# Optimization experiments

Measured on AMD Instinct MI355X. Metric: run time of the kernel, lower is better.

The kernel has to match this reference:

```python
import jax, jax.numpy as jnp
import numpy as np
import math

B, S, D, H = 2, 2048, 1024, 16
DH = D // H  # dim_per_head = 64


def setup_inputs() -> dict:
    key = jax.random.key(0)
    ks = jax.random.split(key, 12)
    s = 1.0 / math.sqrt(D)
    return {
        "key": jax.random.normal(ks[0], (B, S, D), jnp.float32),
        "value": jax.random.normal(ks[1], (B, S, D), jnp.float32),
        "query": jax.random.normal(ks[2], (B, S, D), jnp.float32),
        "mask": jax.random.randint(ks[3], (B, S, S), 0, 2).astype(bool),
        "Wq": jax.random.normal(ks[4], (D, D), jnp.float32) * s,
        "bq": jnp.zeros((D,), jnp.float32),
        "Wk": jax.random.normal(ks[5], (D, D), jnp.float32) * s,
        "bk": jnp.zeros((D,), jnp.float32),
        "Wv": jax.random.normal(ks[6], (D, D), jnp.float32) * s,
        "bv": jnp.zeros((D,), jnp.float32),
        "Wo": jax.random.normal(ks[7], (D, D), jnp.float32) * s,
        "bo": jnp.zeros((D,), jnp.float32),
    }


def _shape(x):
    # [B, S, D] -> [B, H, S, DH]
    return x.reshape(B, -1, H, DH).transpose(0, 2, 1, 3)


def reference(key, value, query, mask, Wq, bq, Wk, bk, Wv, bv, Wo, bo):
    q = _shape(query @ Wq.T + bq)  # [B,H,Sq,DH]
    k = _shape(key @ Wk.T + bk)    # [B,H,Sk,DH]
    v = _shape(value @ Wv.T + bv)  # [B,H,Sk,DH]
    q = q / jnp.sqrt(jnp.asarray(DH, q.dtype))
    scores = jnp.einsum("bhqd,bhkd->bhqk", q, k)
    scores = jnp.where(mask[:, None, :, :], jnp.asarray(-1e18, scores.dtype), scores)
    attn = jax.nn.softmax(scores, axis=-1)
    # dropout is identity in eval/deterministic reference
    ctx = jnp.einsum("bhqk,bhkd->bhqd", attn, v)
    ctx = ctx.transpose(0, 2, 1, 3).reshape(B, -1, D)  # unshape
    return ctx @ Wo.T + bo
```

## Files before the change

kernel.cpp:

```cpp
#include <hip/hip_runtime.h>
#include <math.h>


constexpr int Bc  = 2;
constexpr int Sc  = 2048;
constexpr int Dc  = 1024;
constexpr int Hc  = 16;
constexpr int DHc = 64;
constexpr int BSc = Bc * Sc;

constexpr float LOG2E = 1.4426950408889634f;

typedef __bf16 bf16x8 __attribute__((ext_vector_type(8)));
typedef __bf16 bf16x4 __attribute__((ext_vector_type(4)));
typedef float  f32x4  __attribute__((ext_vector_type(4)));

#define GLDS16(gp, lp) __builtin_amdgcn_global_load_lds( \
    (const __attribute__((address_space(1))) void*)(gp), \
    (__attribute__((address_space(3))) void*)(lp), 16, 0, 0)

__global__ __launch_bounds__(256)
void wsplit(const float* __restrict__ W0, const float* __restrict__ W1,
            const float* __restrict__ W2, const float* __restrict__ W3,
            __bf16* __restrict__ out)
{
    const float* src[4] = {W0, W1, W2, W3};
    const int z = blockIdx.y;
    const size_t idx = ((size_t)blockIdx.x * 256 + threadIdx.x) * 4;
    const float4 v = *(const float4*)&src[z][idx];
    bf16x4 o;
    o[0] = (__bf16)v.x; o[1] = (__bf16)v.y; o[2] = (__bf16)v.z; o[3] = (__bf16)v.w;
    *(bf16x4*)&out[(size_t)z * Dc * Dc + idx] = o;
}

__device__ __forceinline__ void sweep128p(const float* __restrict__ A,
                                          const __bf16* __restrict__ Wh,
                                          char* AsB, char* WsB,
                                          int gm0, int gn0, f32x4 acc[4][4])
{
    const int tid  = threadIdx.x;
    const int w    = tid >> 6;
    const int lane = tid & 63;
    const int cc   = lane & 15;
    const int g    = lane >> 4;
    const int wm   = (w & 1) * 64;
    const int wn   = (w >> 1) * 64;

    int wrow[4], wchk[4];
#pragma unroll
    for (int r = 0; r < 4; ++r) {
        const int L = r * 256 + tid;
        wrow[r] = L >> 3;
        wchk[r] = (L & 7) ^ (wrow[r] & 7);
    }

    float4 av[8];
#pragma unroll
    for (int r = 0; r < 4; ++r)
        GLDS16(Wh + (size_t)(gn0 + wrow[r]) * Dc + wchk[r] * 8,
               WsB + (r * 256 + tid) * 16);
#pragma unroll
    for (int i = 0; i < 8; ++i) {
        const int Lq = i * 256 + tid;
        av[i] = *(const float4*)&A[(size_t)(gm0 + (Lq >> 4)) * Dc + (Lq & 15) * 4];
    }
#pragma unroll
    for (int i = 0; i < 8; ++i) {
        const int Lq = i * 256 + tid;
        const int ar = Lq >> 4, aq = Lq & 15;
        const int off = ar * 128 + ((((aq >> 1) ^ (ar & 7)) << 4) | ((aq & 1) << 3));
        bf16x4 hv;
        hv[0] = (__bf16)av[i].x; hv[1] = (__bf16)av[i].y;
        hv[2] = (__bf16)av[i].z; hv[3] = (__bf16)av[i].w;
        *(bf16x4*)(AsB + off) = hv;
    }

    for (int it = 0; it < Dc / 64; ++it) {
        const char* As = AsB + (it & 1) * 16384;
        const char* Ws = WsB + (it & 1) * 16384;
        __syncthreads();

        const bool more = (it + 1 < Dc / 64);
        if (more) {
            const int kn = (it + 1) * 64;
            char* Wn = WsB + ((it + 1) & 1) * 16384;
#pragma unroll
            for (int r = 0; r < 4; ++r)
                GLDS16(Wh + (size_t)(gn0 + wrow[r]) * Dc + kn + wchk[r] * 8,
                       Wn + (r * 256 + tid) * 16);
#pragma unroll
            for (int i = 0; i < 8; ++i) {
                const int Lq = i * 256 + tid;
                av[i] = *(const float4*)
                    &A[(size_t)(gm0 + (Lq >> 4)) * Dc + kn + (Lq & 15) * 4];
            }
        }

#pragma unroll
        for (int kk = 0; kk < 2; ++kk) {
            const int cb4 = (kk * 4 + g) << 4;
            bf16x8 af[4], bfr[4];
#pragma unroll
            for (int mt = 0; mt < 4; ++mt) {
                const int row = wm + mt * 16 + cc;
                af[mt] = *(const bf16x8*)(As + row * 128 + (cb4 ^ ((row & 7) << 4)));
            }
#pragma unroll
            for (int nt = 0; nt < 4; ++nt) {
                const int row = wn + nt * 16 + cc;
                bfr[nt] = *(const bf16x8*)(Ws + row * 128 + (cb4 ^ ((row & 7) << 4)));
            }
#pragma unroll
            for (int mt = 0; mt < 4; ++mt)
#pragma unroll
                for (int nt = 0; nt < 4; ++nt)
                    acc[mt][nt] = __builtin_amdgcn_mfma_f32_16x16x32_bf16(
                        af[mt], bfr[nt], acc[mt][nt], 0, 0, 0);
        }

        if (more) {
            char* An = AsB + ((it + 1) & 1) * 16384;
#pragma unroll
            for (int i = 0; i < 8; ++i) {
                const int Lq = i * 256 + tid;
                const int ar = Lq >> 4, aq = Lq & 15;
                const int off = ar * 128 +
                                ((((aq >> 1) ^ (ar & 7)) << 4) | ((aq & 1) << 3));
                bf16x4 hv;
                hv[0] = (__bf16)av[i].x; hv[1] = (__bf16)av[i].y;
                hv[2] = (__bf16)av[i].z; hv[3] = (__bf16)av[i].w;
                *(bf16x4*)(An + off) = hv;
            }
        }
    }
}

__device__ __forceinline__ void sweep64p(const __bf16* __restrict__ Ahi,
                                         const __bf16* __restrict__ Alo,
                                         const __bf16* __restrict__ Wh,
                                         char* WsB, char* AhB, char* AlB,
                                         int gm0, int gn0, f32x4 acc[2][4])
{
    const int tid  = threadIdx.x;
    const int w    = tid >> 6;
    const int lane = tid & 63;
    const int cc   = lane & 15;
    const int g    = lane >> 4;
    const int wm   = (w & 1) * 32;
    const int wn   = (w >> 1) * 64;

    int wrow[4], wchk[4];
#pragma unroll
    for (int r = 0; r < 4; ++r) {
        const int L = r * 256 + tid;
        wrow[r] = L >> 3;
        wchk[r] = (L & 7) ^ (wrow[r] & 7);
    }
    int arow[2], achk[2];
#pragma unroll
    for (int r = 0; r < 2; ++r) {
        const int L = r * 256 + tid;
        arow[r] = L >> 3;
        achk[r] = (L & 7) ^ (arow[r] & 7);
    }

#pragma unroll
    for (int r = 0; r < 4; ++r)
        GLDS16(Wh + (size_t)(gn0 + wrow[r]) * Dc + wchk[r] * 8,
               WsB + (r * 256 + tid) * 16);
#pragma unroll
    for (int r = 0; r < 2; ++r) {
        GLDS16(Ahi + (size_t)(gm0 + arow[r]) * Dc + achk[r] * 8,
               AhB + (r * 256 + tid) * 16);
        GLDS16(Alo + (size_t)(gm0 + arow[r]) * Dc + achk[r] * 8,
               AlB + (r * 256 + tid) * 16);
    }

    for (int it = 0; it < Dc / 64; ++it) {
        const char* Ws = WsB + (it & 1) * 16384;
        const char* Ah = AhB + (it & 1) * 8192;
        const char* Al = AlB + (it & 1) * 8192;
        __syncthreads();

        if (it + 1 < Dc / 64) {
            const int kn = (it + 1) * 64;
            char* Wn = WsB + ((it + 1) & 1) * 16384;
            char* Hn = AhB + ((it + 1) & 1) * 8192;
            char* Ln = AlB + ((it + 1) & 1) * 8192;
#pragma unroll
            for (int r = 0; r < 4; ++r)
                GLDS16(Wh + (size_t)(gn0 + wrow[r]) * Dc + kn + wchk[r] * 8,
                       Wn + (r * 256 + tid) * 16);
#pragma unroll
            for (int r = 0; r < 2; ++r) {
                GLDS16(Ahi + (size_t)(gm0 + arow[r]) * Dc + kn + achk[r] * 8,
                       Hn + (r * 256 + tid) * 16);
                GLDS16(Alo + (size_t)(gm0 + arow[r]) * Dc + kn + achk[r] * 8,
                       Ln + (r * 256 + tid) * 16);
            }
        }

#pragma unroll
        for (int kk = 0; kk < 2; ++kk) {
            const int cb4 = (kk * 4 + g) << 4;
            bf16x8 ahi[2], alo[2], bfr[4];
#pragma unroll
            for (int mt = 0; mt < 2; ++mt) {
                const int row = wm + mt * 16 + cc;
                const int off = row * 128 + (cb4 ^ ((row & 7) << 4));
                ahi[mt] = *(const bf16x8*)(Ah + off);
                alo[mt] = *(const bf16x8*)(Al + off);
            }
#pragma unroll
            for (int nt = 0; nt < 4; ++nt) {
                const int row = wn + nt * 16 + cc;
                bfr[nt] = *(const bf16x8*)(Ws + row * 128 + (cb4 ^ ((row & 7) << 4)));
            }
#pragma unroll
            for (int mt = 0; mt < 2; ++mt)
#pragma unroll
                for (int nt = 0; nt < 4; ++nt) {
                    acc[mt][nt] = __builtin_amdgcn_mfma_f32_16x16x32_bf16(
                        ahi[mt], bfr[nt], acc[mt][nt], 0, 0, 0);
                    acc[mt][nt] = __builtin_amdgcn_mfma_f32_16x16x32_bf16(
                        alo[mt], bfr[nt], acc[mt][nt], 0, 0, 0);
                }
        }
    }
}

__global__ __launch_bounds__(256)
void qkv_mfma(const float* __restrict__ query, const float* __restrict__ key,
              const float* __restrict__ value, const __bf16* __restrict__ Whi,
              const float* __restrict__ bq, const float* __restrict__ bk,
              const float* __restrict__ bv,
              __bf16* __restrict__ Qo, __bf16* __restrict__ Ko, __bf16* __restrict__ Vt)
{
    __shared__ __align__(16) char smem[65536];

    const int z = blockIdx.z;
    const float* A    = (z == 0) ? query : (z == 1) ? key : value;
    const float* bias = (z == 0) ? bq    : (z == 1) ? bk  : bv;
    const float scale = (z == 0) ? 0.125f * LOG2E : 1.0f;
    const __bf16* Wh  = Whi + (size_t)z * Dc * Dc;

    const int gm0 = blockIdx.x * 128;
    const int gn0 = blockIdx.y * 128;

    f32x4 acc[4][4];
#pragma unroll
    for (int mt = 0; mt < 4; ++mt)
#pragma unroll
        for (int nt = 0; nt < 4; ++nt) acc[mt][nt] = {0.f, 0.f, 0.f, 0.f};

    sweep128p(A, Wh, smem, smem + 32768, gm0, gn0, acc);

    const int tid = threadIdx.x;
    const int w = tid >> 6, lane = tid & 63;
    const int cc = lane & 15, g = lane >> 4;
    const int wm = (w & 1) * 64, wn = (w >> 1) * 64;

    float bias4[4];
#pragma unroll
    for (int nt = 0; nt < 4; ++nt) bias4[nt] = bias[gn0 + wn + nt * 16 + cc];

    if (z == 2) {
#pragma unroll
        for (int mt = 0; mt < 4; ++mt)
#pragma unroll
            for (int nt = 0; nt < 4; ++nt) {
                const int col = gn0 + wn + nt * 16 + cc;
                const int h = col >> 6, dh = col & 63;
                const int row0 = gm0 + wm + mt * 16 + g * 4;
                const int b = row0 >> 11, s0 = row0 & 2047;
                bf16x4 vv;
#pragma unroll
                for (int reg = 0; reg < 4; ++reg)
                    vv[reg] = (__bf16)(acc[mt][nt][reg] + bias4[nt]);
                *(bf16x4*)&Vt[(((size_t)(b * Hc + h)) * DHc + dh) * Sc + s0] = vv;
            }
    } else {
        __bf16* O = (z == 0) ? Qo : Ko;
#pragma unroll
        for (int mt = 0; mt < 4; ++mt)
#pragma unroll
            for (int nt = 0; nt < 4; ++nt) {
                const int col = gn0 + wn + nt * 16 + cc;
                const int h = col >> 6, dh = col & 63;
#pragma unroll
                for (int reg = 0; reg < 4; ++reg) {
                    const int row = gm0 + wm + mt * 16 + g * 4 + reg;
                    const int b = row >> 11, s = row & 2047;
                    O[(((size_t)(b * Hc + h)) * Sc + s) * DHc + dh] =
                        (__bf16)((acc[mt][nt][reg] + bias4[nt]) * scale);
                }
            }
    }
}

__global__ __launch_bounds__(256)
void out_mfma(const __bf16* __restrict__ ctxHi, const __bf16* __restrict__ ctxLo,
              const __bf16* __restrict__ Wohi,
              const float* __restrict__ bo, float* __restrict__ out)
{
    __shared__ __align__(16) char smem[65536];

    const int gm0 = blockIdx.x * 64;
    const int gn0 = blockIdx.y * 128;

    f32x4 acc[2][4];
#pragma unroll
    for (int mt = 0; mt < 2; ++mt)
#pragma unroll
        for (int nt = 0; nt < 4; ++nt) acc[mt][nt] = {0.f, 0.f, 0.f, 0.f};

    sweep64p(ctxHi, ctxLo, Wohi, smem, smem + 32768, smem + 49152, gm0, gn0, acc);

    const int tid = threadIdx.x;
    const int w = tid >> 6, lane = tid & 63;
    const int cc = lane & 15, g = lane >> 4;
    const int wm = (w & 1) * 32, wn = (w >> 1) * 64;

    float bias4[4];
#pragma unroll
    for (int nt = 0; nt < 4; ++nt) bias4[nt] = bo[gn0 + wn + nt * 16 + cc];

#pragma unroll
    for (int mt = 0; mt < 2; ++mt)
#pragma unroll
        for (int nt = 0; nt < 4; ++nt) {
            const int col = gn0 + wn + nt * 16 + cc;
#pragma unroll
            for (int reg = 0; reg < 4; ++reg) {
                const int row = gm0 + wm + mt * 16 + g * 4 + reg;
                out[(size_t)row * Dc + col] = acc[mt][nt][reg] + bias4[nt];
            }
        }
}

__global__ __launch_bounds__(256)
void mask_pack(const int* __restrict__ mask, unsigned long long* __restrict__ out)
{
    const int lane = threadIdx.x & 63;
    const size_t waveBase = ((size_t)blockIdx.x * 4 + (threadIdx.x >> 6)) * 256;
    unsigned long long b0 = __ballot(mask[waveBase + lane]        != 0);
    unsigned long long b1 = __ballot(mask[waveBase + 64 + lane]   != 0);
    unsigned long long b2 = __ballot(mask[waveBase + 128 + lane]  != 0);
    unsigned long long b3 = __ballot(mask[waveBase + 192 + lane]  != 0);
    if (lane == 0) {
        unsigned long long* dst = out + (waveBase >> 6);
        dst[0] = b0; dst[1] = b1; dst[2] = b2; dst[3] = b3;
    }
}

__global__ __launch_bounds__(256, 2)
void attn_mfma(const __bf16* __restrict__ Q, const __bf16* __restrict__ K,
               const __bf16* __restrict__ Vt,
               const unsigned long long* __restrict__ mp,
               __bf16* __restrict__ ctxHi, __bf16* __restrict__ ctxLo)
{
    __shared__ __align__(16) char smem[40960];

    const int tid  = threadIdx.x;
    const int w    = tid >> 6;
    const int lane = tid & 63;
    const int cc   = lane & 15;
    const int g    = lane >> 4;
    const int bh   = blockIdx.y;
    const int b    = bh >> 4;
    const int h    = bh & 15;
    const int qw   = blockIdx.x * 128 + w * 32;

    const __bf16* Qb  = Q  + (size_t)bh * Sc * DHc;
    const __bf16* Kb  = K  + (size_t)bh * Sc * DHc;
    const __bf16* Vtb = Vt + (size_t)bh * DHc * Sc;

    char* Pw = smem + 32768 + w * 2048;

    bf16x8 qa[2][2];
#pragma unroll
    for (int mt = 0; mt < 2; ++mt) {
        qa[mt][0] = *(const bf16x8*)&Qb[(size_t)(qw + mt * 16 + cc) * DHc + g * 8];
        qa[mt][1] = *(const bf16x8*)&Qb[(size_t)(qw + mt * 16 + cc) * DHc + 32 + g * 8];
    }

    f32x4 o[2][4] = {};
    float l[2][4] = {};

    const int ci[2] = {tid, 256 + tid};
    int  rowi[2], ski[2];
#pragma unroll
    for (int i = 0; i < 2; ++i) {
        rowi[i] = ci[i] >> 3;
        const int sl = ci[i] & 7;
        ski[i] = sl ^ (rowi[i] & 7);
    }

#pragma unroll
    for (int i = 0; i < 2; ++i) {
        GLDS16(Kb + (size_t)rowi[i] * DHc + ski[i] * 8,
               smem + ci[i] * 16);
        GLDS16(Vtb + (size_t)rowi[i] * Sc + ski[i] * 8,
               smem + 8192 + ci[i] * 16);
    }

    for (int it = 0; it < 32; ++it) {
        const int k0 = it * 64;
        char* Ks = smem + (it & 1) * 16384;
        char* Vs = Ks + 8192;

        __syncthreads();

        if (it + 1 < 32) {
            char* Kn = smem + ((it + 1) & 1) * 16384;
            const int kn = k0 + 64;
#pragma unroll
            for (int i = 0; i < 2; ++i) {
                GLDS16(Kb + (size_t)(kn + rowi[i]) * DHc + ski[i] * 8,
                       Kn + ci[i] * 16);
                GLDS16(Vtb + (size_t)rowi[i] * Sc + kn + ski[i] * 8,
                       Kn + 8192 + ci[i] * 16);
            }
        }

        unsigned long long mw[2][4];
#pragma unroll
        for (int mt = 0; mt < 2; ++mt)
#pragma unroll
            for (int r = 0; r < 4; ++r)
                mw[mt][r] = mp[(size_t)(b * Sc + qw + mt * 16 + g * 4 + r) * (Sc / 64)
                               + (k0 >> 6)];

        f32x4 sc[2][4];
#pragma unroll
        for (int nt = 0; nt < 4; ++nt) {
            const int row = nt * 16 + cc;
            const int rx  = (row & 7) << 4;
            const bf16x8 kb0 = *(const bf16x8*)(Ks + row * 128 + ((g << 4) ^ rx));
            const bf16x8 kb1 = *(const bf16x8*)(Ks + row * 128 + ((64 + (g << 4)) ^ rx));
            f32x4 z0 = {-24.f, -24.f, -24.f, -24.f};
            z0 = __builtin_amdgcn_mfma_f32_16x16x32_bf16(qa[0][0], kb0, z0, 0, 0, 0);
            z0 = __builtin_amdgcn_mfma_f32_16x16x32_bf16(qa[0][1], kb1, z0, 0, 0, 0);
            sc[0][nt] = z0;
            f32x4 z1 = {-24.f, -24.f, -24.f, -24.f};
            z1 = __builtin_amdgcn_mfma_f32_16x16x32_bf16(qa[1][0], kb0, z1, 0, 0, 0);
            z1 = __builtin_amdgcn_mfma_f32_16x16x32_bf16(qa[1][1], kb1, z1, 0, 0, 0);
            sc[1][nt] = z1;
        }

        bf16x8 pa[2][2];
#pragma unroll
        for (int mt = 0; mt < 2; ++mt) {
            unsigned mlo[4], mhi[4];
#pragma unroll
            for (int r = 0; r < 4; ++r) {
                const unsigned long long sh = mw[mt][r] >> cc;
                mlo[r] = (unsigned)sh;
                mhi[r] = (unsigned)(sh >> 32);
            }
#pragma unroll
            for (int nt = 0; nt < 4; ++nt)
#pragma unroll
                for (int r = 0; r < 4; ++r) {
                    float p = __builtin_amdgcn_exp2f(sc[mt][nt][r]);
                    const unsigned bit =
                        (nt == 0) ? (mlo[r] & 1u) :
                        (nt == 1) ? (mlo[r] & 0x10000u) :
                        (nt == 2) ? (mhi[r] & 1u) : (mhi[r] & 0x10000u);
                    p = bit ? 0.f : p;
                    l[mt][r] += p;
                    *(__bf16*)(Pw + (g * 4 + r) * 128 +
                               (((nt ^ g) << 5) | (cc << 1))) = (__bf16)p;
                }
            const int sw = (cc >> 2) << 5;
            pa[mt][0] = *(const bf16x8*)(Pw + cc * 128 + ((g * 16) ^ sw));
            pa[mt][1] = *(const bf16x8*)(Pw + cc * 128 + ((64 + g * 16) ^ sw));
        }

#pragma unroll
        for (int nt = 0; nt < 4; ++nt) {
            const int row = nt * 16 + cc;
            const int rx  = (row & 7) << 4;
            const bf16x8 vb0 = *(const bf16x8*)(Vs + row * 128 + ((g << 4) ^ rx));
            const bf16x8 vb1 = *(const bf16x8*)(Vs + row * 128 + ((64 + (g << 4)) ^ rx));
            o[0][nt] = __builtin_amdgcn_mfma_f32_16x16x32_bf16(pa[0][0], vb0, o[0][nt], 0, 0, 0);
            o[0][nt] = __builtin_amdgcn_mfma_f32_16x16x32_bf16(pa[0][1], vb1, o[0][nt], 0, 0, 0);
            o[1][nt] = __builtin_amdgcn_mfma_f32_16x16x32_bf16(pa[1][0], vb0, o[1][nt], 0, 0, 0);
            o[1][nt] = __builtin_amdgcn_mfma_f32_16x16x32_bf16(pa[1][1], vb1, o[1][nt], 0, 0, 0);
        }
    }

#pragma unroll
    for (int off = 1; off < 16; off <<= 1)
#pragma unroll
        for (int mt = 0; mt < 2; ++mt)
#pragma unroll
            for (int r = 0; r < 4; ++r)
                l[mt][r] += __shfl_xor(l[mt][r], off, 16);

#pragma unroll
    for (int mt = 0; mt < 2; ++mt)
#pragma unroll
        for (int r = 0; r < 4; ++r) {
            const float inv = 1.0f / l[mt][r];
            const int q = qw + mt * 16 + g * 4 + r;
#pragma unroll
            for (int nt = 0; nt < 4; ++nt) {
                const size_t idx = ((size_t)b * Sc + q) * Dc + h * 64 + nt * 16 + cc;
                const float v = o[mt][nt][r] * inv;
                const __bf16 hi = (__bf16)v;
                ctxHi[idx] = hi;
                ctxLo[idx] = (__bf16)(v - (float)hi);
            }
        }
}

extern "C" void kernel_launch(void* const* d_in, const int* in_sizes, int n_in,
                              void* d_out, int out_size, void* d_ws, size_t ws_size,
                              hipStream_t stream)
{
    const float* key   = (const float*)d_in[0];
    const float* value = (const float*)d_in[1];
    const float* query = (const float*)d_in[2];
    const int*   mask  = (const int*)  d_in[3];
    const float* Wq    = (const float*)d_in[4];
    const float* bq    = (const float*)d_in[5];
    const float* Wk    = (const float*)d_in[6];
    const float* bk    = (const float*)d_in[7];
    const float* Wv    = (const float*)d_in[8];
    const float* bv    = (const float*)d_in[9];
    const float* Wo    = (const float*)d_in[10];
    const float* bo    = (const float*)d_in[11];
    float* out = (float*)d_out;

    char* wsb = (char*)d_ws;
    __bf16* Qbf  = (__bf16*)(wsb);
    __bf16* Kbf  = (__bf16*)(wsb + ((size_t)8  << 20));
    __bf16* Vt   = (__bf16*)(wsb + ((size_t)16 << 20));
    unsigned long long* mpk = (unsigned long long*)(wsb + ((size_t)32 << 20));
    __bf16* Whi  = (__bf16*)(wsb + ((size_t)33 << 20));
    __bf16* ctxHi = (__bf16*)(wsb + ((size_t)41 << 20));
    __bf16* ctxLo = (__bf16*)(wsb + ((size_t)49 << 20));

    dim3 gws(Dc * Dc / (256 * 4), 4);
    wsplit<<<gws, 256, 0, stream>>>(Wq, Wk, Wv, Wo, Whi);

    dim3 gqkv(BSc / 128, Dc / 128, 3);
    qkv_mfma<<<gqkv, 256, 0, stream>>>(query, key, value, Whi, bq, bk, bv,
                                       Qbf, Kbf, Vt);

    const int mask_n = Bc * Sc * Sc;
    mask_pack<<<mask_n / 1024, 256, 0, stream>>>(mask, mpk);

    dim3 gattn(Sc / 128, Bc * Hc);
    attn_mfma<<<gattn, 256, 0, stream>>>(Qbf, Kbf, Vt, mpk, ctxHi, ctxLo);

    dim3 gout(BSc / 64, Dc / 128);
    out_mfma<<<gout, 256, 0, stream>>>(ctxHi, ctxLo, Whi + (size_t)3 * Dc * Dc,
                                       bo, out);
}
```

Before: 273.2 us.

## Fuse all stages into one persistent kernel with software grid barriers

Replaces the five separate launches (weight cast, QKV projection, mask pack, attention, output projection) with one persistent kernel of 512 blocks. The blocks loop over the old grids and are separated by an atomic-counter grid barrier. This is meant to remove launch gaps and tail idle time between kernels. In exchange, every block must be co-resident (launch bounds of 2 blocks per CU with 64KB of shared memory), the attention phase now runs with 64KB of LDS instead of 40KB, and the barriers spin on atomics.

After: 629.3 us. 130% more time.

```diff
diff --git a/kernel.cpp b/kernel.cpp
--- a/kernel.cpp
+++ b/kernel.cpp
@@ -19,18 +19,28 @@
     (const __attribute__((address_space(1))) void*)(gp), \
     (__attribute__((address_space(3))) void*)(lp), 16, 0, 0)
 
-__global__ __launch_bounds__(256)
-void wsplit(const float* __restrict__ W0, const float* __restrict__ W1,
-            const float* __restrict__ W2, const float* __restrict__ W3,
-            __bf16* __restrict__ out)
-{
-    const float* src[4] = {W0, W1, W2, W3};
-    const int z = blockIdx.y;
-    const size_t idx = ((size_t)blockIdx.x * 256 + threadIdx.x) * 4;
-    const float4 v = *(const float4*)&src[z][idx];
-    bf16x4 o;
-    o[0] = (__bf16)v.x; o[1] = (__bf16)v.y; o[2] = (__bf16)v.z; o[3] = (__bf16)v.w;
-    *(bf16x4*)&out[(size_t)z * Dc * Dc + idx] = o;
+__device__ __forceinline__ void grid_sync(unsigned* cnt, unsigned* gen, unsigned nb)
+{
+    __syncthreads();
+    if (threadIdx.x == 0) {
+        __threadfence();
+        const unsigned g = __hip_atomic_load(gen, __ATOMIC_RELAXED,
+                                             __HIP_MEMORY_SCOPE_AGENT);
+        const unsigned prev = __hip_atomic_fetch_add(cnt, 1u, __ATOMIC_ACQ_REL,
+                                                     __HIP_MEMORY_SCOPE_AGENT);
+        if (prev == nb - 1) {
+            __hip_atomic_store(cnt, 0u, __ATOMIC_RELAXED,
+                               __HIP_MEMORY_SCOPE_AGENT);
+            __hip_atomic_fetch_add(gen, 1u, __ATOMIC_ACQ_REL,
+                                   __HIP_MEMORY_SCOPE_AGENT);
+        } else {
+            while (__hip_atomic_load(gen, __ATOMIC_ACQUIRE,
+                                     __HIP_MEMORY_SCOPE_AGENT) == g)
+                __builtin_amdgcn_s_sleep(8);
+        }
+        __threadfence();
+    }
+    __syncthreads();
 }
 
 __device__ __forceinline__ void sweep128p(const float* __restrict__ A,
@@ -229,23 +239,19 @@
     }
 }
 
-__global__ __launch_bounds__(256)
-void qkv_mfma(const float* __restrict__ query, const float* __restrict__ key,
-              const float* __restrict__ value, const __bf16* __restrict__ Whi,
-              const float* __restrict__ bq, const float* __restrict__ bk,
-              const float* __restrict__ bv,
-              __bf16* __restrict__ Qo, __bf16* __restrict__ Ko, __bf16* __restrict__ Vt)
-{
-    __shared__ __align__(16) char smem[65536];
-
-    const int z = blockIdx.z;
-    const float* A    = (z == 0) ? query : (z == 1) ? key : value;
-    const float* bias = (z == 0) ? bq    : (z == 1) ? bk  : bv;
-    const float scale = (z == 0) ? 0.125f * LOG2E : 1.0f;
-    const __bf16* Wh  = Whi + (size_t)z * Dc * Dc;
-
-    const int gm0 = blockIdx.x * 128;
-    const int gn0 = blockIdx.y * 128;
+__device__ void phase_qkv(int bx, int by, int bz, char* smem,
+                          const float* query, const float* key, const float* value,
+                          const __bf16* Whi, const float* bq, const float* bk,
+                          const float* bv,
+                          __bf16* Qo, __bf16* Ko, __bf16* Vt)
+{
+    const float* A    = (bz == 0) ? query : (bz == 1) ? key : value;
+    const float* bias = (bz == 0) ? bq    : (bz == 1) ? bk  : bv;
+    const float scale = (bz == 0) ? 0.125f * LOG2E : 1.0f;
+    const __bf16* Wh  = Whi + (size_t)bz * Dc * Dc;
+
+    const int gm0 = bx * 128;
+    const int gn0 = by * 128;
 
     f32x4 acc[4][4];
 #pragma unroll
@@ -264,7 +270,7 @@
 #pragma unroll
     for (int nt = 0; nt < 4; ++nt) bias4[nt] = bias[gn0 + wn + nt * 16 + cc];
 
-    if (z == 2) {
+    if (bz == 2) {
 #pragma unroll
         for (int mt = 0; mt < 4; ++mt)
 #pragma unroll
@@ -280,7 +286,7 @@
                 *(bf16x4*)&Vt[(((size_t)(b * Hc + h)) * DHc + dh) * Sc + s0] = vv;
             }
     } else {
-        __bf16* O = (z == 0) ? Qo : Ko;
+        __bf16* O = (bz == 0) ? Qo : Ko;
 #pragma unroll
         for (int mt = 0; mt < 4; ++mt)
 #pragma unroll
@@ -298,78 +304,20 @@
     }
 }
 
-__global__ __launch_bounds__(256)
-void out_mfma(const __bf16* __restrict__ ctxHi, const __bf16* __restrict__ ctxLo,
-              const __bf16* __restrict__ Wohi,
-              const float* __restrict__ bo, float* __restrict__ out)
-{
-    __shared__ __align__(16) char smem[65536];
-
-    const int gm0 = blockIdx.x * 64;
-    const int gn0 = blockIdx.y * 128;
-
-    f32x4 acc[2][4];
-#pragma unroll
-    for (int mt = 0; mt < 2; ++mt)
-#pragma unroll
-        for (int nt = 0; nt < 4; ++nt) acc[mt][nt] = {0.f, 0.f, 0.f, 0.f};
-
-    sweep64p(ctxHi, ctxLo, Wohi, smem, smem + 32768, smem + 49152, gm0, gn0, acc);
-
-    const int tid = threadIdx.x;
-    const int w = tid >> 6, lane = tid & 63;
-    const int cc = lane & 15, g = lane >> 4;
-    const int wm = (w & 1) * 32, wn = (w >> 1) * 64;
-
-    float bias4[4];
-#pragma unroll
-    for (int nt = 0; nt < 4; ++nt) bias4[nt] = bo[gn0 + wn + nt * 16 + cc];
-
-#pragma unroll
-    for (int mt = 0; mt < 2; ++mt)
-#pragma unroll
-        for (int nt = 0; nt < 4; ++nt) {
-            const int col = gn0 + wn + nt * 16 + cc;
-#pragma unroll
-            for (int reg = 0; reg < 4; ++reg) {
-                const int row = gm0 + wm + mt * 16 + g * 4 + reg;
-                out[(size_t)row * Dc + col] = acc[mt][nt][reg] + bias4[nt];
-            }
-        }
-}
-
-__global__ __launch_bounds__(256)
-void mask_pack(const int* __restrict__ mask, unsigned long long* __restrict__ out)
-{
-    const int lane = threadIdx.x & 63;
-    const size_t waveBase = ((size_t)blockIdx.x * 4 + (threadIdx.x >> 6)) * 256;
-    unsigned long long b0 = __ballot(mask[waveBase + lane]        != 0);
-    unsigned long long b1 = __ballot(mask[waveBase + 64 + lane]   != 0);
-    unsigned long long b2 = __ballot(mask[waveBase + 128 + lane]  != 0);
-    unsigned long long b3 = __ballot(mask[waveBase + 192 + lane]  != 0);
-    if (lane == 0) {
-        unsigned long long* dst = out + (waveBase >> 6);
-        dst[0] = b0; dst[1] = b1; dst[2] = b2; dst[3] = b3;
-    }
-}
-
-__global__ __launch_bounds__(256, 2)
-void attn_mfma(const __bf16* __restrict__ Q, const __bf16* __restrict__ K,
-               const __bf16* __restrict__ Vt,
-               const unsigned long long* __restrict__ mp,
-               __bf16* __restrict__ ctxHi, __bf16* __restrict__ ctxLo)
-{
-    __shared__ __align__(16) char smem[40960];
-
+__device__ void phase_attn(int bx, int by, char* smem,
+                           const __bf16* Q, const __bf16* K, const __bf16* Vt,
+                           const unsigned long long* mp,
+                           __bf16* ctxHi, __bf16* ctxLo)
+{
     const int tid  = threadIdx.x;
     const int w    = tid >> 6;
     const int lane = tid & 63;
     const int cc   = lane & 15;
     const int g    = lane >> 4;
-    const int bh   = blockIdx.y;
+    const int bh   = by;
     const int b    = bh >> 4;
     const int h    = bh & 15;
-    const int qw   = blockIdx.x * 128 + w * 32;
+    const int qw   = bx * 128 + w * 32;
 
     const __bf16* Qb  = Q  + (size_t)bh * Sc * DHc;
     const __bf16* Kb  = K  + (size_t)bh * Sc * DHc;
@@ -398,10 +346,8 @@
 
 #pragma unroll
     for (int i = 0; i < 2; ++i) {
-        GLDS16(Kb + (size_t)rowi[i] * DHc + ski[i] * 8,
-               smem + ci[i] * 16);
-        GLDS16(Vtb + (size_t)rowi[i] * Sc + ski[i] * 8,
-               smem + 8192 + ci[i] * 16);
+        GLDS16(Kb + (size_t)rowi[i] * DHc + ski[i] * 8, smem + ci[i] * 16);
+        GLDS16(Vtb + (size_t)rowi[i] * Sc + ski[i] * 8, smem + 8192 + ci[i] * 16);
     }
 
     for (int it = 0; it < 32; ++it) {
@@ -515,6 +461,101 @@
         }
 }
 
+__device__ void phase_out(int bx, int by, char* smem,
+                          const __bf16* ctxHi, const __bf16* ctxLo,
+                          const __bf16* Wohi, const float* bo, float* out)
+{
+    const int gm0 = bx * 64;
+    const int gn0 = by * 128;
+
+    f32x4 acc[2][4];
+#pragma unroll
+    for (int mt = 0; mt < 2; ++mt)
+#pragma unroll
+        for (int nt = 0; nt < 4; ++nt) acc[mt][nt] = {0.f, 0.f, 0.f, 0.f};
+
+    sweep64p(ctxHi, ctxLo, Wohi, smem, smem + 32768, smem + 49152, gm0, gn0, acc);
+
+    const int tid = threadIdx.x;
+    const int w = tid >> 6, lane = tid & 63;
+    const int cc = lane & 15, g = lane >> 4;
+    const int wm = (w & 1) * 32, wn = (w >> 1) * 64;
+
+    float bias4[4];
+#pragma unroll
+    for (int nt = 0; nt < 4; ++nt) bias4[nt] = bo[gn0 + wn + nt * 16 + cc];
+
+#pragma unroll
+    for (int mt = 0; mt < 2; ++mt)
+#pragma unroll
+        for (int nt = 0; nt < 4; ++nt) {
+            const int col = gn0 + wn + nt * 16 + cc;
+#pragma unroll
+            for (int reg = 0; reg < 4; ++reg) {
+                const int row = gm0 + wm + mt * 16 + g * 4 + reg;
+                out[(size_t)row * Dc + col] = acc[mt][nt][reg] + bias4[nt];
+            }
+        }
+}
+
+__global__ __launch_bounds__(256, 2)
+void fused_mha(const float* __restrict__ query, const float* __restrict__ key,
+               const float* __restrict__ value, const int* __restrict__ mask,
+               const float* __restrict__ Wq, const float* __restrict__ bq,
+               const float* __restrict__ Wk, const float* __restrict__ bk,
+               const float* __restrict__ Wv, const float* __restrict__ bv,
+               const float* __restrict__ Wo, const float* __restrict__ bo,
+               __bf16* __restrict__ Qbf, __bf16* __restrict__ Kbf,
+               __bf16* __restrict__ Vt, unsigned long long* __restrict__ mpk,
+               __bf16* __restrict__ Whi, __bf16* __restrict__ ctxHi,
+               __bf16* __restrict__ ctxLo, float* __restrict__ out,
+               unsigned* __restrict__ bar)
+{
+    __shared__ __align__(16) char smem[65536];
+    const unsigned nb = gridDim.x;
+    const int bid = blockIdx.x;
+    const int tid = threadIdx.x;
+    unsigned* cnt = bar;
+    unsigned* gen = bar + 16;
+
+    {
+        const float* src[4] = {Wq, Wk, Wv, Wo};
+        for (int t = bid; t < 4096; t += nb) {
+            const int x = t & 1023, z = t >> 10;
+            const size_t idx = ((size_t)x * 256 + tid) * 4;
+            const float4 v = *(const float4*)&src[z][idx];
+            bf16x4 o;
+            o[0] = (__bf16)v.x; o[1] = (__bf16)v.y;
+            o[2] = (__bf16)v.z; o[3] = (__bf16)v.w;
+            *(bf16x4*)&Whi[(size_t)z * Dc * Dc + idx] = o;
+        }
+        const int lane = tid & 63;
+        for (int t = bid; t < 8192; t += nb) {
+            const size_t waveBase = ((size_t)t * 4 + (tid >> 6)) * 256;
+            unsigned long long b0 = __ballot(mask[waveBase + lane]       != 0);
+            unsigned long long b1 = __ballot(mask[waveBase + 64 + lane]  != 0);
+            unsigned long long b2 = __ballot(mask[waveBase + 128 + lane] != 0);
+            unsigned long long b3 = __ballot(mask[waveBase + 192 + lane] != 0);
+            if (lane == 0) {
+                unsigned long long* dst = mpk + (waveBase >> 6);
+                dst[0] = b0; dst[1] = b1; dst[2] = b2; dst[3] = b3;
+            }
+        }
+    }
+    grid_sync(cnt, gen, nb);
+
+    for (int t = bid; t < 768; t += nb)
+        phase_qkv(t & 31, (t >> 5) & 7, t >> 8, smem,
+                  query, key, value, Whi, bq, bk, bv, Qbf, Kbf, Vt);
+    grid_sync(cnt, gen, nb);
+
+    phase_attn(bid & 15, bid >> 4, smem, Qbf, Kbf, Vt, mpk, ctxHi, ctxLo);
+    grid_sync(cnt, gen, nb);
+
+    phase_out(bid & 63, bid >> 6, smem, ctxHi, ctxLo,
+              Whi + (size_t)3 * Dc * Dc, bo, out);
+}
+
 extern "C" void kernel_launch(void* const* d_in, const int* in_sizes, int n_in,
                               void* d_out, int out_size, void* d_ws, size_t ws_size,
                               hipStream_t stream)
@@ -534,28 +575,19 @@
     float* out = (float*)d_out;
 
     char* wsb = (char*)d_ws;
-    __bf16* Qbf  = (__bf16*)(wsb);
-    __bf16* Kbf  = (__bf16*)(wsb + ((size_t)8  << 20));
-    __bf16* Vt   = (__bf16*)(wsb + ((size_t)16 << 20));
+    __bf16* Qbf   = (__bf16*)(wsb);
+    __bf16* Kbf   = (__bf16*)(wsb + ((size_t)8  << 20));
+    __bf16* Vt    = (__bf16*)(wsb + ((size_t)16 << 20));
     unsigned long long* mpk = (unsigned long long*)(wsb + ((size_t)32 << 20));
-    __bf16* Whi  = (__bf16*)(wsb + ((size_t)33 << 20));
+    __bf16* Whi   = (__bf16*)(wsb + ((size_t)33 << 20));
     __bf16* ctxHi = (__bf16*)(wsb + ((size_t)41 << 20));
     __bf16* ctxLo = (__bf16*)(wsb + ((size_t)49 << 20));
-
-    dim3 gws(Dc * Dc / (256 * 4), 4);
-    wsplit<<<gws, 256, 0, stream>>>(Wq, Wk, Wv, Wo, Whi);
-
-    dim3 gqkv(BSc / 128, Dc / 128, 3);
-    qkv_mfma<<<gqkv, 256, 0, stream>>>(query, key, value, Whi, bq, bk, bv,
-                                       Qbf, Kbf, Vt);
-
-    const int mask_n = Bc * Sc * Sc;
-    mask_pack<<<mask_n / 1024, 256, 0, stream>>>(mask, mpk);
-
-    dim3 gattn(Sc / 128, Bc * Hc);
-    attn_mfma<<<gattn, 256, 0, stream>>>(Qbf, Kbf, Vt, mpk, ctxHi, ctxLo);
-
-    dim3 gout(BSc / 64, Dc / 128);
-    out_mfma<<<gout, 256, 0, stream>>>(ctxHi, ctxLo, Whi + (size_t)3 * Dc * Dc,
-                                       bo, out);
-}
+    unsigned* bar = (unsigned*)(wsb + ((size_t)58 << 20));
+
+    hipMemsetAsync(bar, 0, 128, stream);
+
+    fused_mha<<<512, 256, 0, stream>>>(query, key, value, mask,
+                                       Wq, bq, Wk, bk, Wv, bv, Wo, bo,
+                                       Qbf, Kbf, Vt, mpk, Whi,
+                                       ctxHi, ctxLo, out, bar);
+}
```
